# Kernel tuning notes

Measured on AMD Instinct MI355X. Metric: run time of the kernel, lower is better.

The kernel has to match this reference:

```python
import jax, jax.numpy as jnp
import numpy as np

B, S, D, H = 2, 2048, 1024, 16
DK = D // H  # 64
EPS = 1e-10
ROPE_BASE = 500000.0


def _rms_norm(x, w):
    # RMSNorm over last dim: w * x / sqrt(mean(x^2) + eps)
    return w * x * jax.lax.rsqrt(jnp.mean(x * x, axis=-1, keepdims=True) + EPS)


def _rope_tables(seq_len, dk):
    inv_freq = 1.0 / (ROPE_BASE ** (jnp.arange(0, dk, 2, dtype=jnp.float32) / dk))
    t = jnp.arange(seq_len, dtype=jnp.float32)
    freqs = jnp.outer(t, inv_freq)            # (S, dk/2)
    emb = jnp.concatenate([freqs, freqs], -1)  # (S, dk)
    return jnp.cos(emb), jnp.sin(emb)


def _rotate_half(x):
    x1, x2 = jnp.split(x, 2, axis=-1)
    return jnp.concatenate([-x2, x1], axis=-1)


def setup_inputs() -> dict:
    key = jax.random.key(0)
    ks = jax.random.split(key, 8)
    scale = 1.0 / np.sqrt(D)
    return {
        "q": jax.random.normal(ks[0], (B, S, D), jnp.float32),
        "k": jax.random.normal(ks[1], (B, S, D), jnp.float32),
        "v": jax.random.normal(ks[2], (B, S, D), jnp.float32),
        "Wq": jax.random.normal(ks[3], (D, D), jnp.float32) * scale,
        "Wk": jax.random.normal(ks[4], (D, D), jnp.float32) * scale,
        "Wv": jax.random.normal(ks[5], (D, D), jnp.float32) * scale,
        "Wo": jax.random.normal(ks[6], (D, D), jnp.float32) * scale,
        "q_norm_w": jnp.ones((DK,), jnp.float32) + 0.02 * jax.random.normal(ks[7], (DK,), jnp.float32),
        "k_norm_w": jnp.ones((DK,), jnp.float32),
    }


def reference(q, k, v, Wq, Wk, Wv, Wo, q_norm_w, k_norm_w):
    Bq, Sq, _ = q.shape
    # Projections (torch Linear: x @ W.T), split into heads -> (B, H, S, DK)
    def proj(x, W):
        return (x @ W.T).reshape(Bq, Sq, H, DK).transpose(0, 2, 1, 3)
    query, key_, value = proj(q, Wq), proj(k, Wk), proj(v, Wv)
    # Per-head QK RMSNorm
    query = _rms_norm(query, q_norm_w)
    key_ = _rms_norm(key_, k_norm_w)
    # RoPE
    cos, sin = _rope_tables(Sq, DK)  # (S, DK) each; broadcast over (B, H)
    query = query * cos + _rotate_half(query) * sin
    key_ = key_ * cos + _rotate_half(key_) * sin
    # Causal attention
    scale = 1.0 / np.sqrt(DK)
    scores = jnp.einsum("bhqd,bhkd->bhqk", query, key_) * scale
    causal = jnp.tril(jnp.ones((Sq, Sq), bool))
    scores = jnp.where(causal, scores, -jnp.inf)
    probs = jax.nn.softmax(scores, axis=-1)
    attn = jnp.einsum("bhqk,bhkd->bhqd", probs, value)
    # Merge heads and output projection
    attn = attn.transpose(0, 2, 1, 3).reshape(Bq, Sq, D)
    return attn @ Wo.T
```

## Files before the change

### kernel.cpp

```cpp
#include <hip/hip_runtime.h>
#include <hip/hip_bf16.h>
#include <math.h>

#define B_  2
#define S_  2048
#define D_  1024
#define H_  16
#define DK_ 64

typedef __attribute__((ext_vector_type(8))) short bf16x8;
typedef __attribute__((ext_vector_type(4))) float f32x4;

#define MFMA_BF16(a, b, c) __builtin_amdgcn_mfma_f32_16x16x32_bf16((a), (b), (c), 0, 0, 0)

#define QSCALE 0.18033688011112042f
#define ROPE_L2 0.591611512f

__device__ __forceinline__ unsigned short f2bf(float f) {
  unsigned int u = __float_as_uint(f);
  u += 0x7FFFu + ((u >> 16) & 1u);
  return (unsigned short)(u >> 16);
}

__device__ __forceinline__ void gl_lds16(const void* g, void* l) {
  __builtin_amdgcn_global_load_lds(
      (const __attribute__((address_space(1))) void*)g,
      (__attribute__((address_space(3))) void*)l, 16, 0, 0);
}

__device__ __forceinline__ int lsw(int row, int col) {
  return row * 64 + ((((col) >> 3) ^ (row & 7)) << 3) + (col & 7);
}

__global__ __launch_bounds__(256)
void cvt_bf16(const float* __restrict__ q, const float* __restrict__ k,
              const float* __restrict__ v, const float* __restrict__ wq,
              const float* __restrict__ wk, const float* __restrict__ wv,
              const float* __restrict__ wo,
              unsigned short* __restrict__ qb, unsigned short* __restrict__ kb,
              unsigned short* __restrict__ vb, unsigned short* __restrict__ wqb,
              unsigned short* __restrict__ wkb, unsigned short* __restrict__ wvb,
              unsigned short* __restrict__ wob) {
  const float* src; unsigned short* dst; int n;
  switch (blockIdx.y) {
    case 0: src = q;  dst = qb;  n = B_ * S_ * D_; break;
    case 1: src = k;  dst = kb;  n = B_ * S_ * D_; break;
    case 2: src = v;  dst = vb;  n = B_ * S_ * D_; break;
    case 3: src = wq; dst = wqb; n = D_ * D_; break;
    case 4: src = wk; dst = wkb; n = D_ * D_; break;
    case 5: src = wv; dst = wvb; n = D_ * D_; break;
    default: src = wo; dst = wob; n = D_ * D_; break;
  }
  const int i = (blockIdx.x * 256 + threadIdx.x) * 4;
  if (i >= n) return;
  float4 val = *(const float4*)&src[i];
  ushort4 r4;
  r4.x = f2bf(val.x); r4.y = f2bf(val.y); r4.z = f2bf(val.z); r4.w = f2bf(val.w);
  *(ushort4*)&dst[i] = r4;
}

__global__ __launch_bounds__(256)
void gemm_qkv(const unsigned short* __restrict__ qa, const unsigned short* __restrict__ ka,
              const unsigned short* __restrict__ va,
              const unsigned short* __restrict__ wq, const unsigned short* __restrict__ wk,
              const unsigned short* __restrict__ wv,
              unsigned short* __restrict__ Qo, unsigned short* __restrict__ Ko,
              unsigned short* __restrict__ Vo,
              const float* __restrict__ qnw, const float* __restrict__ knw) {
  __shared__ unsigned short As[2][128 * 32];
  __shared__ unsigned short Bs[2][128 * 32];
  const int z = blockIdx.z;
  const unsigned short* A = (z == 0) ? qa : (z == 1) ? ka : va;
  const unsigned short* W = (z == 0) ? wq : (z == 1) ? wk : wv;
  unsigned short* out     = (z == 0) ? Qo : (z == 1) ? Ko : Vo;

  const int t = threadIdx.x, lane = t & 63, wave = t >> 6;
  const int l16 = lane & 15, quad = lane >> 4;
  const int wm = wave >> 1, wn = wave & 1;
  const int m0 = blockIdx.y * 128, j0 = blockIdx.x * 128;

  f32x4 acc[4][4];
#pragma unroll
  for (int i = 0; i < 4; ++i)
#pragma unroll
    for (int j = 0; j < 4; ++j) acc[i][j] = (f32x4)(0.0f);

  auto stage = [&](int kb, int buf) {
#pragma unroll
    for (int i = 0; i < 2; ++i) {
      const int c  = (wave * 2 + i) * 64 + lane;
      const int r  = c >> 2;
      const int co = (c & 3) * 8;
      gl_lds16(&A[(size_t)(m0 + r) * D_ + kb + co], &As[buf][(wave * 2 + i) * 512]);
      gl_lds16(&W[(size_t)(j0 + r) * D_ + kb + co], &Bs[buf][(wave * 2 + i) * 512]);
    }
  };

  stage(0, 0);
  for (int kb = 0; kb < D_; kb += 32) {
    const int buf = (kb >> 5) & 1;
    __syncthreads();
    if (kb + 32 < D_) stage(kb + 32, buf ^ 1);

    bf16x8 af[4], bfr[4];
#pragma unroll
    for (int mi = 0; mi < 4; ++mi)
      af[mi] = *(const bf16x8*)&As[buf][(wm * 64 + mi * 16 + l16) * 32 + quad * 8];
#pragma unroll
    for (int ni = 0; ni < 4; ++ni)
      bfr[ni] = *(const bf16x8*)&Bs[buf][(wn * 64 + ni * 16 + l16) * 32 + quad * 8];
#pragma unroll
    for (int mi = 0; mi < 4; ++mi)
#pragma unroll
      for (int ni = 0; ni < 4; ++ni)
        acc[mi][ni] = MFMA_BF16(af[mi], bfr[ni], acc[mi][ni]);
  }

  const int h = blockIdx.x * 2 + wn;
  if (z == 2) {
#pragma unroll
    for (int mi = 0; mi < 4; ++mi) {
      const int rowb = m0 + wm * 64 + mi * 16 + quad * 4;
#pragma unroll
      for (int ni = 0; ni < 4; ++ni) {
        const int dk = ni * 16 + l16;
#pragma unroll
        for (int r = 0; r < 4; ++r) {
          const int rr = rowb + r;
          const int b = rr >> 11, s = rr & (S_ - 1);
          out[((size_t)(b * H_ + h) * S_ + s) * DK_ + dk] = f2bf(acc[mi][ni][r]);
        }
      }
    }
  } else {
    const float* nw = (z == 0) ? qnw : knw;
    const float sc  = (z == 0) ? QSCALE : 1.0f;
    float wv_[4];
#pragma unroll
    for (int ni = 0; ni < 4; ++ni) wv_[ni] = nw[ni * 16 + l16];
    const float invA = exp2f(-(float)l16 * ROPE_L2);
    const float invB = exp2f(-(float)(16 + l16) * ROPE_L2);
#pragma unroll
    for (int mi = 0; mi < 4; ++mi) {
#pragma unroll
      for (int r = 0; r < 4; ++r) {
        const int rowg = m0 + wm * 64 + mi * 16 + quad * 4 + r;
        const int b = rowg >> 11, s = rowg & (S_ - 1);
        float ss = 0.f;
#pragma unroll
        for (int ni = 0; ni < 4; ++ni) ss += acc[mi][ni][r] * acc[mi][ni][r];
#pragma unroll
        for (int m = 1; m < 16; m <<= 1) ss += __shfl_xor(ss, m);
        const float rms = rsqrtf(ss * (1.0f / DK_) + 1e-10f);
        float xn[4];
#pragma unroll
        for (int ni = 0; ni < 4; ++ni) xn[ni] = wv_[ni] * acc[mi][ni][r] * rms;
        const float fA = (float)s * invA, fB = (float)s * invB;
        const float cA = __cosf(fA) * sc, sA = __sinf(fA) * sc;
        const float cB = __cosf(fB) * sc, sB = __sinf(fB) * sc;
        float o0 = xn[0] * cA - xn[2] * sA;
        float o1 = xn[1] * cB - xn[3] * sB;
        float o2 = xn[2] * cA + xn[0] * sA;
        float o3 = xn[3] * cB + xn[1] * sB;
        const size_t base = ((size_t)(b * H_ + h) * S_ + s) * DK_;
        out[base +  0 + l16] = f2bf(o0);
        out[base + 16 + l16] = f2bf(o1);
        out[base + 32 + l16] = f2bf(o2);
        out[base + 48 + l16] = f2bf(o3);
      }
    }
  }
}

__global__ __launch_bounds__(256)
void transpose_v(const unsigned short* __restrict__ Vh, unsigned short* __restrict__ Vt) {
  __shared__ unsigned short tile[64 * 65];
  const int bh = blockIdx.y, s0 = blockIdx.x * 64;
  const int t = threadIdx.x;
  const size_t base = (size_t)bh * S_ * DK_;
#pragma unroll
  for (int i = 0; i < 2; ++i) {
    const int c = i * 256 + t;
    const int r = c >> 3, co = (c & 7) * 8;
    unsigned short tmp[8];
    *(bf16x8*)tmp = *(const bf16x8*)&Vh[base + (size_t)(s0 + r) * DK_ + co];
#pragma unroll
    for (int jj = 0; jj < 8; ++jj) tile[r * 65 + co + jj] = tmp[jj];
  }
  __syncthreads();
#pragma unroll
  for (int i = 0; i < 2; ++i) {
    const int c = i * 256 + t;
    const int dk = c >> 3, so = (c & 7) * 8;
    unsigned short tmp[8];
#pragma unroll
    for (int jj = 0; jj < 8; ++jj) tmp[jj] = tile[(so + jj) * 65 + dk];
    *(bf16x8*)&Vt[(size_t)bh * DK_ * S_ + (size_t)dk * S_ + s0 + so] = *(bf16x8*)tmp;
  }
}

__global__ __launch_bounds__(256)
void flash2(const unsigned short* __restrict__ Q, const unsigned short* __restrict__ K,
            const unsigned short* __restrict__ Vt, unsigned short* __restrict__ Oa) {
  __shared__ unsigned short Ks[2][64 * 64];
  __shared__ unsigned short Vs[2][64 * 64];
  __shared__ unsigned short Ps[128 * 64];
  const int bx = blockIdx.x;
  const int qt = (bx < 256) ? (bx >> 5) : (15 - ((bx - 256) >> 5));
  const int bh = bx & 31;
  const int t = threadIdx.x, lane = t & 63, wave = t >> 6;
  const int l16 = lane & 15, quad = lane >> 4;
  const size_t hb = (size_t)bh * S_ * DK_;
  const unsigned short* Qh  = Q + hb;
  const unsigned short* Kh  = K + hb;
  const unsigned short* Vth = Vt + hb;

  bf16x8 qf[2][2];
#pragma unroll
  for (int mi = 0; mi < 2; ++mi)
#pragma unroll
    for (int ks = 0; ks < 2; ++ks)
      qf[mi][ks] = *(const bf16x8*)
        &Qh[(size_t)(qt * 128 + wave * 32 + mi * 16 + l16) * DK_ + ks * 32 + quad * 8];

  bf16x8 ones;
#pragma unroll
  for (int j = 0; j < 8; ++j) ones[j] = (short)0x3F80;

  f32x4 o[2][4], lacc[2];
#pragma unroll
  for (int mi = 0; mi < 2; ++mi) {
    lacc[mi] = (f32x4)(0.0f);
#pragma unroll
    for (int ni = 0; ni < 4; ++ni) o[mi][ni] = (f32x4)(0.0f);
  }

  auto stage = [&](int kt, int bufi) {
#pragma unroll
    for (int i = 0; i < 2; ++i) {
      const int rbase = wave * 16 + i * 8;
      const int r = rbase + (lane >> 3);
      const int c = ((lane & 7) ^ (r & 7)) * 8;
      gl_lds16(&Kh[(size_t)(kt * 64 + r) * DK_ + c], &Ks[bufi][rbase * 64]);
      gl_lds16(&Vth[(size_t)r * S_ + kt * 64 + c], &Vs[bufi][rbase * 64]);
    }
  };

  const int nkt = 2 * qt + 2;
  stage(0, 0);
  for (int kt = 0; kt < nkt; ++kt) {
    const int buf = kt & 1;
    __syncthreads();
    if (kt + 1 < nkt) stage(kt + 1, buf ^ 1);

    f32x4 sv[4][2];
#pragma unroll
    for (int kvi = 0; kvi < 4; ++kvi)
#pragma unroll
      for (int mi = 0; mi < 2; ++mi) sv[kvi][mi] = (f32x4)(0.0f);
#pragma unroll
    for (int ks = 0; ks < 2; ++ks) {
      bf16x8 ak[4];
#pragma unroll
      for (int kvi = 0; kvi < 4; ++kvi)
        ak[kvi] = *(const bf16x8*)&Ks[buf][lsw(kvi * 16 + l16, ks * 32 + quad * 8)];
#pragma unroll
      for (int kvi = 0; kvi < 4; ++kvi)
#pragma unroll
        for (int mi = 0; mi < 2; ++mi)
          sv[kvi][mi] = MFMA_BF16(ak[kvi], qf[mi][ks], sv[kvi][mi]);
    }

    const bool diag = (kt >= 2 * qt);
#pragma unroll
    for (int kvi = 0; kvi < 4; ++kvi)
#pragma unroll
      for (int mi = 0; mi < 2; ++mi) {
        const int qg  = qt * 128 + wave * 32 + mi * 16 + l16;
        const int kvb = kt * 64 + kvi * 16 + quad * 4;
        float p[4];
#pragma unroll
        for (int r = 0; r < 4; ++r) {
          float x = sv[kvi][mi][r];
          if (diag && (kvb + r) > qg) x = -INFINITY;
          p[r] = exp2f(x);
        }
        const unsigned int d0 =
            (__float_as_uint(p[1]) & 0xFFFF0000u) | (__float_as_uint(p[0]) >> 16);
        const unsigned int d1 =
            (__float_as_uint(p[3]) & 0xFFFF0000u) | (__float_as_uint(p[2]) >> 16);
        *(uint2*)&Ps[lsw(wave * 32 + mi * 16 + l16, kvi * 16 + quad * 4)] =
            make_uint2(d0, d1);
      }
    asm volatile("s_waitcnt lgkmcnt(0)" ::: "memory");

#pragma unroll
    for (int ks = 0; ks < 2; ++ks) {
      bf16x8 ap[2], bv[4];
#pragma unroll
      for (int mi = 0; mi < 2; ++mi)
        ap[mi] = *(const bf16x8*)&Ps[lsw(wave * 32 + mi * 16 + l16, ks * 32 + quad * 8)];
#pragma unroll
      for (int ni = 0; ni < 4; ++ni)
        bv[ni] = *(const bf16x8*)&Vs[buf][lsw(ni * 16 + l16, ks * 32 + quad * 8)];
#pragma unroll
      for (int mi = 0; mi < 2; ++mi) {
#pragma unroll
        for (int ni = 0; ni < 4; ++ni)
          o[mi][ni] = MFMA_BF16(ap[mi], bv[ni], o[mi][ni]);
        lacc[mi] = MFMA_BF16(ap[mi], ones, lacc[mi]);
      }
    }
  }

  const int b = bh >> 4, h = bh & 15;
#pragma unroll
  for (int mi = 0; mi < 2; ++mi)
#pragma unroll
    for (int r = 0; r < 4; ++r) {
      const int srow = qt * 128 + wave * 32 + mi * 16 + quad * 4 + r;
      const float linv = 1.0f / lacc[mi][r];
#pragma unroll
      for (int ni = 0; ni < 4; ++ni)
        Oa[((size_t)(b * S_ + srow) * H_ + h) * DK_ + ni * 16 + l16] =
            f2bf(o[mi][ni][r] * linv);
    }
}

__global__ __launch_bounds__(256)
void gemm_out(const unsigned short* __restrict__ A, const unsigned short* __restrict__ W,
              float* __restrict__ out) {
  __shared__ unsigned short As[2][128 * 32];
  __shared__ unsigned short Bs[2][128 * 32];
  const int t = threadIdx.x, lane = t & 63, wave = t >> 6;
  const int l16 = lane & 15, quad = lane >> 4;
  const int wm = wave >> 1, wn = wave & 1;
  const int m0 = blockIdx.y * 128, j0 = blockIdx.x * 128;

  f32x4 acc[4][4];
#pragma unroll
  for (int i = 0; i < 4; ++i)
#pragma unroll
    for (int j = 0; j < 4; ++j) acc[i][j] = (f32x4)(0.0f);

  auto stage = [&](int kb, int buf) {
#pragma unroll
    for (int i = 0; i < 2; ++i) {
      const int c  = (wave * 2 + i) * 64 + lane;
      const int r  = c >> 2;
      const int co = (c & 3) * 8;
      gl_lds16(&A[(size_t)(m0 + r) * D_ + kb + co], &As[buf][(wave * 2 + i) * 512]);
      gl_lds16(&W[(size_t)(j0 + r) * D_ + kb + co], &Bs[buf][(wave * 2 + i) * 512]);
    }
  };

  stage(0, 0);
  for (int kb = 0; kb < D_; kb += 32) {
    const int buf = (kb >> 5) & 1;
    __syncthreads();
    if (kb + 32 < D_) stage(kb + 32, buf ^ 1);

    bf16x8 af[4], bfr[4];
#pragma unroll
    for (int mi = 0; mi < 4; ++mi)
      af[mi] = *(const bf16x8*)&As[buf][(wm * 64 + mi * 16 + l16) * 32 + quad * 8];
#pragma unroll
    for (int ni = 0; ni < 4; ++ni)
      bfr[ni] = *(const bf16x8*)&Bs[buf][(wn * 64 + ni * 16 + l16) * 32 + quad * 8];
#pragma unroll
    for (int mi = 0; mi < 4; ++mi)
#pragma unroll
      for (int ni = 0; ni < 4; ++ni)
        acc[mi][ni] = MFMA_BF16(af[mi], bfr[ni], acc[mi][ni]);
  }

#pragma unroll
  for (int mi = 0; mi < 4; ++mi) {
    const int rowb = m0 + wm * 64 + mi * 16 + quad * 4;
#pragma unroll
    for (int ni = 0; ni < 4; ++ni) {
      const int col = j0 + wn * 64 + ni * 16 + l16;
#pragma unroll
      for (int r = 0; r < 4; ++r)
        out[(size_t)(rowb + r) * D_ + col] = acc[mi][ni][r];
    }
  }
}

extern "C" void kernel_launch(void* const* d_in, const int* in_sizes, int n_in,
                              void* d_out, int out_size, void* d_ws, size_t ws_size,
                              hipStream_t stream) {
  (void)in_sizes; (void)n_in; (void)out_size; (void)ws_size;
  const float* q  = (const float*)d_in[0];
  const float* k  = (const float*)d_in[1];
  const float* v  = (const float*)d_in[2];
  const float* Wq = (const float*)d_in[3];
  const float* Wk = (const float*)d_in[4];
  const float* Wv = (const float*)d_in[5];
  const float* Wo = (const float*)d_in[6];
  const float* qw = (const float*)d_in[7];
  const float* kw = (const float*)d_in[8];

  char* ws = (char*)d_ws;
  const size_t MB = 1u << 20;
  unsigned short* qb  = (unsigned short*)(ws + 0 * MB);
  unsigned short* kb  = (unsigned short*)(ws + 8 * MB);
  unsigned short* vb  = (unsigned short*)(ws + 16 * MB);
  unsigned short* wqb = (unsigned short*)(ws + 24 * MB);
  unsigned short* wkb = (unsigned short*)(ws + 26 * MB);
  unsigned short* wvb = (unsigned short*)(ws + 28 * MB);
  unsigned short* wob = (unsigned short*)(ws + 30 * MB);
  unsigned short* Qb  = (unsigned short*)(ws + 32 * MB);
  unsigned short* Kb  = (unsigned short*)(ws + 40 * MB);
  unsigned short* Vh  = (unsigned short*)(ws + 48 * MB);
  unsigned short* Vtb = (unsigned short*)(ws + 56 * MB);
  unsigned short* Ab  = (unsigned short*)(ws + 64 * MB);

  cvt_bf16<<<dim3(4096, 7), 256, 0, stream>>>(q, k, v, Wq, Wk, Wv, Wo,
                                              qb, kb, vb, wqb, wkb, wvb, wob);

  gemm_qkv<<<dim3(D_ / 128, (B_ * S_) / 128, 3), 256, 0, stream>>>(
      qb, kb, vb, wqb, wkb, wvb, Qb, Kb, Vh, qw, kw);

  transpose_v<<<dim3(S_ / 64, B_ * H_), 256, 0, stream>>>(Vh, Vtb);

  flash2<<<512, 256, 0, stream>>>(Qb, Kb, Vtb, Ab);

  gemm_out<<<dim3(D_ / 128, (B_ * S_) / 128), 256, 0, stream>>>(Ab, wob, (float*)d_out);
}
```

Baseline: 239.8 us.

## Fuse V transpose into QKV GEMM epilogue and shrink flash tiles to 64 rows

The V projection epilogue now writes V directly in transposed (dk-major) layout with packed 4-element stores, so the separate transpose_v kernel and its intermediate buffer go away. The attention kernel now processes 64 query rows per block instead of 128, with one 16-row slice per wave. That doubles the grid to 1024 blocks with causal pairing of q tiles, and splits the diagonal-masked tile from the unmasked path. The change removes one launch and a full round trip of V through memory and improves load balance, but halves K/V reuse per block and doubles K/V tile loads.

```diff
diff --git a/kernel.cpp b/kernel.cpp
--- a/kernel.cpp
+++ b/kernel.cpp
@@ -65,14 +65,13 @@
               const unsigned short* __restrict__ wq, const unsigned short* __restrict__ wk,
               const unsigned short* __restrict__ wv,
               unsigned short* __restrict__ Qo, unsigned short* __restrict__ Ko,
-              unsigned short* __restrict__ Vo,
+              unsigned short* __restrict__ Vto,
               const float* __restrict__ qnw, const float* __restrict__ knw) {
   __shared__ unsigned short As[2][128 * 32];
   __shared__ unsigned short Bs[2][128 * 32];
   const int z = blockIdx.z;
   const unsigned short* A = (z == 0) ? qa : (z == 1) ? ka : va;
   const unsigned short* W = (z == 0) ? wq : (z == 1) ? wk : wv;
-  unsigned short* out     = (z == 0) ? Qo : (z == 1) ? Ko : Vo;
 
   const int t = threadIdx.x, lane = t & 63, wave = t >> 6;
   const int l16 = lane & 15, quad = lane >> 4;
@@ -121,18 +120,19 @@
 #pragma unroll
     for (int mi = 0; mi < 4; ++mi) {
       const int rowb = m0 + wm * 64 + mi * 16 + quad * 4;
+      const int b = rowb >> 11, s0 = rowb & (S_ - 1);
 #pragma unroll
       for (int ni = 0; ni < 4; ++ni) {
         const int dk = ni * 16 + l16;
-#pragma unroll
-        for (int r = 0; r < 4; ++r) {
-          const int rr = rowb + r;
-          const int b = rr >> 11, s = rr & (S_ - 1);
-          out[((size_t)(b * H_ + h) * S_ + s) * DK_ + dk] = f2bf(acc[mi][ni][r]);
-        }
+        const unsigned int u0 =
+            (unsigned int)f2bf(acc[mi][ni][0]) | ((unsigned int)f2bf(acc[mi][ni][1]) << 16);
+        const unsigned int u1 =
+            (unsigned int)f2bf(acc[mi][ni][2]) | ((unsigned int)f2bf(acc[mi][ni][3]) << 16);
+        *(uint2*)&Vto[((size_t)((b * H_ + h) * DK_ + dk)) * S_ + s0] = make_uint2(u0, u1);
       }
     }
   } else {
+    unsigned short* out = (z == 0) ? Qo : Ko;
     const float* nw = (z == 0) ? qnw : knw;
     const float sc  = (z == 0) ? QSCALE : 1.0f;
     float wv_[4];
@@ -173,40 +173,14 @@
 }
 
 __global__ __launch_bounds__(256)
-void transpose_v(const unsigned short* __restrict__ Vh, unsigned short* __restrict__ Vt) {
-  __shared__ unsigned short tile[64 * 65];
-  const int bh = blockIdx.y, s0 = blockIdx.x * 64;
-  const int t = threadIdx.x;
-  const size_t base = (size_t)bh * S_ * DK_;
-#pragma unroll
-  for (int i = 0; i < 2; ++i) {
-    const int c = i * 256 + t;
-    const int r = c >> 3, co = (c & 7) * 8;
-    unsigned short tmp[8];
-    *(bf16x8*)tmp = *(const bf16x8*)&Vh[base + (size_t)(s0 + r) * DK_ + co];
-#pragma unroll
-    for (int jj = 0; jj < 8; ++jj) tile[r * 65 + co + jj] = tmp[jj];
-  }
-  __syncthreads();
-#pragma unroll
-  for (int i = 0; i < 2; ++i) {
-    const int c = i * 256 + t;
-    const int dk = c >> 3, so = (c & 7) * 8;
-    unsigned short tmp[8];
-#pragma unroll
-    for (int jj = 0; jj < 8; ++jj) tmp[jj] = tile[(so + jj) * 65 + dk];
-    *(bf16x8*)&Vt[(size_t)bh * DK_ * S_ + (size_t)dk * S_ + s0 + so] = *(bf16x8*)tmp;
-  }
-}
-
-__global__ __launch_bounds__(256)
-void flash2(const unsigned short* __restrict__ Q, const unsigned short* __restrict__ K,
+void flash3(const unsigned short* __restrict__ Q, const unsigned short* __restrict__ K,
             const unsigned short* __restrict__ Vt, unsigned short* __restrict__ Oa) {
   __shared__ unsigned short Ks[2][64 * 64];
   __shared__ unsigned short Vs[2][64 * 64];
-  __shared__ unsigned short Ps[128 * 64];
+  __shared__ unsigned short Ps[64 * 64];
   const int bx = blockIdx.x;
-  const int qt = (bx < 256) ? (bx >> 5) : (15 - ((bx - 256) >> 5));
+  const int idx = bx >> 5;
+  const int qt = (idx < 16) ? idx : (47 - idx);
   const int bh = bx & 31;
   const int t = threadIdx.x, lane = t & 63, wave = t >> 6;
   const int l16 = lane & 15, quad = lane >> 4;
@@ -215,25 +189,20 @@
   const unsigned short* Kh  = K + hb;
   const unsigned short* Vth = Vt + hb;
 
-  bf16x8 qf[2][2];
-#pragma unroll
-  for (int mi = 0; mi < 2; ++mi)
-#pragma unroll
-    for (int ks = 0; ks < 2; ++ks)
-      qf[mi][ks] = *(const bf16x8*)
-        &Qh[(size_t)(qt * 128 + wave * 32 + mi * 16 + l16) * DK_ + ks * 32 + quad * 8];
+  bf16x8 qf[2];
+#pragma unroll
+  for (int ks = 0; ks < 2; ++ks)
+    qf[ks] = *(const bf16x8*)
+      &Qh[(size_t)(qt * 64 + wave * 16 + l16) * DK_ + ks * 32 + quad * 8];
 
   bf16x8 ones;
 #pragma unroll
   for (int j = 0; j < 8; ++j) ones[j] = (short)0x3F80;
 
-  f32x4 o[2][4], lacc[2];
-#pragma unroll
-  for (int mi = 0; mi < 2; ++mi) {
-    lacc[mi] = (f32x4)(0.0f);
-#pragma unroll
-    for (int ni = 0; ni < 4; ++ni) o[mi][ni] = (f32x4)(0.0f);
-  }
+  f32x4 o[4], lacc;
+  lacc = (f32x4)(0.0f);
+#pragma unroll
+  for (int ni = 0; ni < 4; ++ni) o[ni] = (f32x4)(0.0f);
 
   auto stage = [&](int kt, int bufi) {
 #pragma unroll
@@ -246,18 +215,16 @@
     }
   };
 
-  const int nkt = 2 * qt + 2;
+  const int nkt = qt + 1;
   stage(0, 0);
   for (int kt = 0; kt < nkt; ++kt) {
     const int buf = kt & 1;
     __syncthreads();
     if (kt + 1 < nkt) stage(kt + 1, buf ^ 1);
 
-    f32x4 sv[4][2];
-#pragma unroll
-    for (int kvi = 0; kvi < 4; ++kvi)
-#pragma unroll
-      for (int mi = 0; mi < 2; ++mi) sv[kvi][mi] = (f32x4)(0.0f);
+    f32x4 sv[4];
+#pragma unroll
+    for (int kvi = 0; kvi < 4; ++kvi) sv[kvi] = (f32x4)(0.0f);
 #pragma unroll
     for (int ks = 0; ks < 2; ++ks) {
       bf16x8 ak[4];
@@ -266,65 +233,61 @@
         ak[kvi] = *(const bf16x8*)&Ks[buf][lsw(kvi * 16 + l16, ks * 32 + quad * 8)];
 #pragma unroll
       for (int kvi = 0; kvi < 4; ++kvi)
-#pragma unroll
-        for (int mi = 0; mi < 2; ++mi)
-          sv[kvi][mi] = MFMA_BF16(ak[kvi], qf[mi][ks], sv[kvi][mi]);
-    }
-
-    const bool diag = (kt >= 2 * qt);
-#pragma unroll
-    for (int kvi = 0; kvi < 4; ++kvi)
-#pragma unroll
-      for (int mi = 0; mi < 2; ++mi) {
-        const int qg  = qt * 128 + wave * 32 + mi * 16 + l16;
-        const int kvb = kt * 64 + kvi * 16 + quad * 4;
-        float p[4];
+        sv[kvi] = MFMA_BF16(ak[kvi], qf[ks], sv[kvi]);
+    }
+
+    float p[4][4];
+    if (kt == qt) {
+      const int qg = qt * 64 + wave * 16 + l16;
+#pragma unroll
+      for (int kvi = 0; kvi < 4; ++kvi)
 #pragma unroll
         for (int r = 0; r < 4; ++r) {
-          float x = sv[kvi][mi][r];
-          if (diag && (kvb + r) > qg) x = -INFINITY;
-          p[r] = exp2f(x);
+          float x = sv[kvi][r];
+          if ((kt * 64 + kvi * 16 + quad * 4 + r) > qg) x = -INFINITY;
+          p[kvi][r] = exp2f(x);
         }
-        const unsigned int d0 =
-            (__float_as_uint(p[1]) & 0xFFFF0000u) | (__float_as_uint(p[0]) >> 16);
-        const unsigned int d1 =
-            (__float_as_uint(p[3]) & 0xFFFF0000u) | (__float_as_uint(p[2]) >> 16);
-        *(uint2*)&Ps[lsw(wave * 32 + mi * 16 + l16, kvi * 16 + quad * 4)] =
-            make_uint2(d0, d1);
-      }
+    } else {
+#pragma unroll
+      for (int kvi = 0; kvi < 4; ++kvi)
+#pragma unroll
+        for (int r = 0; r < 4; ++r) p[kvi][r] = exp2f(sv[kvi][r]);
+    }
+
+#pragma unroll
+    for (int kvi = 0; kvi < 4; ++kvi) {
+      const unsigned int d0 =
+          (__float_as_uint(p[kvi][1]) & 0xFFFF0000u) | (__float_as_uint(p[kvi][0]) >> 16);
+      const unsigned int d1 =
+          (__float_as_uint(p[kvi][3]) & 0xFFFF0000u) | (__float_as_uint(p[kvi][2]) >> 16);
+      *(uint2*)&Ps[lsw(wave * 16 + l16, kvi * 16 + quad * 4)] = make_uint2(d0, d1);
+    }
     asm volatile("s_waitcnt lgkmcnt(0)" ::: "memory");
 
 #pragma unroll
     for (int ks = 0; ks < 2; ++ks) {
-      bf16x8 ap[2], bv[4];
-#pragma unroll
-      for (int mi = 0; mi < 2; ++mi)
-        ap[mi] = *(const bf16x8*)&Ps[lsw(wave * 32 + mi * 16 + l16, ks * 32 + quad * 8)];
+      bf16x8 ap, bv[4];
+      ap = *(const bf16x8*)&Ps[lsw(wave * 16 + l16, ks * 32 + quad * 8)];
 #pragma unroll
       for (int ni = 0; ni < 4; ++ni)
         bv[ni] = *(const bf16x8*)&Vs[buf][lsw(ni * 16 + l16, ks * 32 + quad * 8)];
 #pragma unroll
-      for (int mi = 0; mi < 2; ++mi) {
-#pragma unroll
-        for (int ni = 0; ni < 4; ++ni)
-          o[mi][ni] = MFMA_BF16(ap[mi], bv[ni], o[mi][ni]);
-        lacc[mi] = MFMA_BF16(ap[mi], ones, lacc[mi]);
-      }
+      for (int ni = 0; ni < 4; ++ni)
+        o[ni] = MFMA_BF16(ap, bv[ni], o[ni]);
+      lacc = MFMA_BF16(ap, ones, lacc);
     }
   }
 
   const int b = bh >> 4, h = bh & 15;
 #pragma unroll
-  for (int mi = 0; mi < 2; ++mi)
-#pragma unroll
-    for (int r = 0; r < 4; ++r) {
-      const int srow = qt * 128 + wave * 32 + mi * 16 + quad * 4 + r;
-      const float linv = 1.0f / lacc[mi][r];
-#pragma unroll
-      for (int ni = 0; ni < 4; ++ni)
-        Oa[((size_t)(b * S_ + srow) * H_ + h) * DK_ + ni * 16 + l16] =
-            f2bf(o[mi][ni][r] * linv);
-    }
+  for (int r = 0; r < 4; ++r) {
+    const int srow = qt * 64 + wave * 16 + quad * 4 + r;
+    const float linv = 1.0f / lacc[r];
+#pragma unroll
+    for (int ni = 0; ni < 4; ++ni)
+      Oa[((size_t)(b * S_ + srow) * H_ + h) * DK_ + ni * 16 + l16] =
+          f2bf(o[ni][r] * linv);
+  }
 }
 
 __global__ __launch_bounds__(256)
@@ -412,19 +375,16 @@
   unsigned short* wob = (unsigned short*)(ws + 30 * MB);
   unsigned short* Qb  = (unsigned short*)(ws + 32 * MB);
   unsigned short* Kb  = (unsigned short*)(ws + 40 * MB);
-  unsigned short* Vh  = (unsigned short*)(ws + 48 * MB);
-  unsigned short* Vtb = (unsigned short*)(ws + 56 * MB);
-  unsigned short* Ab  = (unsigned short*)(ws + 64 * MB);
+  unsigned short* Vtb = (unsigned short*)(ws + 48 * MB);
+  unsigned short* Ab  = (unsigned short*)(ws + 56 * MB);
 
   cvt_bf16<<<dim3(4096, 7), 256, 0, stream>>>(q, k, v, Wq, Wk, Wv, Wo,
                                               qb, kb, vb, wqb, wkb, wvb, wob);
 
   gemm_qkv<<<dim3(D_ / 128, (B_ * S_) / 128, 3), 256, 0, stream>>>(
-      qb, kb, vb, wqb, wkb, wvb, Qb, Kb, Vh, qw, kw);
-
-  transpose_v<<<dim3(S_ / 64, B_ * H_), 256, 0, stream>>>(Vh, Vtb);
-
-  flash2<<<512, 256, 0, stream>>>(Qb, Kb, Vtb, Ab);
+      qb, kb, vb, wqb, wkb, wvb, Qb, Kb, Vtb, qw, kw);
+
+  flash3<<<1024, 256, 0, stream>>>(Qb, Kb, Vtb, Ab);
 
   gemm_out<<<dim3(D_ / 128, (B_ * S_) / 128), 256, 0, stream>>>(Ab, wob, (float*)d_out);
 }
```

Result: faster. 215.3 us (-10.2%).
